# Kernel optimization log

Measured on AMD Instinct MI355X. Metric: run time of the kernel, lower is better.

Reference implementation:

```python
import jax, jax.numpy as jnp
import numpy as np

N_STATE = 1024
N_HEAD = 16
D_HEAD = N_STATE // N_HEAD  # 64
B, T = 4, 4096


def _linear(x, W, b=None):
    # x: (B,C,T,1), W: (O,C) == 1x1 conv2d over channel dim
    y = jnp.einsum('oc,bctx->botx', W, x)
    if b is not None:
        y = y + b[None, :, None, None]
    return y


def _phi(x):
    return jax.nn.silu(x) + 1.0


def setup_inputs() -> dict:
    key = jax.random.key(0)
    ks = jax.random.split(key, 8)
    s = 1.0 / np.sqrt(N_STATE).astype(np.float32)
    x = jax.random.normal(ks[0], (B, N_STATE, T, 1), jnp.float32)
    Wq = jax.random.normal(ks[1], (N_STATE, N_STATE), jnp.float32) * s
    bq = jax.random.normal(ks[2], (N_STATE,), jnp.float32) * s
    Wk = jax.random.normal(ks[3], (N_STATE, N_STATE), jnp.float32) * s
    Wv = jax.random.normal(ks[4], (N_STATE, N_STATE), jnp.float32) * s
    bv = jax.random.normal(ks[5], (N_STATE,), jnp.float32) * s
    Wo = jax.random.normal(ks[6], (N_STATE, N_STATE), jnp.float32) * s
    bo = jax.random.normal(ks[7], (N_STATE,), jnp.float32) * s
    return {"x": x, "Wq": Wq, "bq": bq, "Wk": Wk, "Wv": Wv, "bv": bv, "Wo": Wo, "bo": bo}


def reference(x, Wq, bq, Wk, Wv, bv, Wo, bo):
    Bb, C, Tt, _ = x.shape
    H, Dh = N_HEAD, D_HEAD
    q = _linear(x, Wq, bq)
    k = _linear(x, Wk)          # key has no bias
    v = _linear(x, Wv, bv)
    # (B, C, T, 1) -> (B, H, Dh, T, 1); C = H*Dh so reshape matches torch
    phi_q = _phi(q).reshape(Bb, H, Dh, Tt, 1)
    phi_k = _phi(k).reshape(Bb, H, Dh, Tt, 1)
    v = v.reshape(Bb, H, Dh, Tt, 1)
    k_sum = jnp.cumsum(phi_k, axis=3)
    kv_sum = jnp.cumsum(phi_k * v, axis=3)
    den = jnp.sum(phi_q * k_sum, axis=2, keepdims=True) + 1e-6
    out = (phi_q * kv_sum / den).reshape(Bb, C, Tt, 1)
    out = out / np.sqrt(Dh).astype(np.float32)
    return _linear(out, Wo, bo)
```

## Files before the change

### kernel.cpp

```cpp
#include <hip/hip_runtime.h>
#include <hip/hip_bf16.h>
#include <stdint.h>

#define T_SEQ 4096
#define C_ST  1024
#define K2    2048
#define K3    3072
#define NB    4
#define NCHUNK 128
#define CHUNK  32

typedef __bf16 bf16x8_t __attribute__((ext_vector_type(8)));
typedef float f32x4_t __attribute__((ext_vector_type(4)));
typedef unsigned short u16x8 __attribute__((ext_vector_type(8)));
typedef unsigned short u16x4 __attribute__((ext_vector_type(4)));
typedef __attribute__((address_space(1))) unsigned int as1u32;
typedef __attribute__((address_space(3))) unsigned int as3u32;

__device__ __forceinline__ unsigned short bfbits(float f) {
  __hip_bfloat16 h = __float2bfloat16(f);
  return *reinterpret_cast<unsigned short*>(&h);
}
__device__ __forceinline__ float bf2f(unsigned short u) {
  __hip_bfloat16 h;
  *reinterpret_cast<unsigned short*>(&h) = u;
  return __bfloat162float(h);
}
__device__ __forceinline__ float phi_f(float x) {
  return x / (1.0f + __expf(-x)) + 1.0f;
}

__global__ __launch_bounds__(256) void conv_w_kernel(
    const float* __restrict__ Wq, const float* __restrict__ Wk,
    const float* __restrict__ Wv, const float* __restrict__ Wo,
    unsigned short* __restrict__ W3, unsigned short* __restrict__ Wo3) {
  int r = blockIdx.x;
  int which = blockIdx.y;
  const float* src = (which == 0) ? Wq : (which == 1) ? Wk : (which == 2) ? Wv : Wo;
  unsigned short* dst = (which < 3) ? (W3 + (size_t)(which * 1024 + r) * K2)
                                    : (Wo3 + (size_t)r * K2);
  int c4 = threadIdx.x * 4;
  float4 v = *reinterpret_cast<const float4*>(&src[(size_t)r * 1024 + c4]);
  float fe[4] = {v.x, v.y, v.z, v.w};
  u16x4 hh;
#pragma unroll
  for (int e = 0; e < 4; ++e) hh[e] = bfbits(fe[e]);
  *reinterpret_cast<u16x4*>(&dst[c4])        = hh;
  *reinterpret_cast<u16x4*>(&dst[1024 + c4]) = hh;
}

__global__ __launch_bounds__(256) void conv_x_kernel(
    const float* __restrict__ x0, unsigned short* __restrict__ xT0) {
  __shared__ float tile[64][65];
  int c0 = blockIdx.y * 64, t0 = blockIdx.x * 64, z = blockIdx.z;
  const float* xb = x0 + (size_t)z * C_ST * T_SEQ + (size_t)c0 * T_SEQ + t0;
  unsigned short* xT = xT0 + (size_t)z * T_SEQ * K2;
  int tid = threadIdx.x;
#pragma unroll
  for (int p = 0; p < 4; ++p) {
    int idx = tid + p * 256;
    int r = idx >> 4, q4 = (idx & 15) * 4;
    float4 v = *reinterpret_cast<const float4*>(&xb[(size_t)r * T_SEQ + q4]);
    tile[r][q4 + 0] = v.x; tile[r][q4 + 1] = v.y;
    tile[r][q4 + 2] = v.z; tile[r][q4 + 3] = v.w;
  }
  __syncthreads();
  int r = tid >> 2, q = (tid & 3) * 16;
  u16x8 h0, h1, l0, l1;
#pragma unroll
  for (int j = 0; j < 8; ++j) {
    float f = tile[q + j][r];
    unsigned short hb = bfbits(f);
    h0[j] = hb; l0[j] = bfbits(f - bf2f(hb));
  }
#pragma unroll
  for (int j = 0; j < 8; ++j) {
    float f = tile[q + 8 + j][r];
    unsigned short hb = bfbits(f);
    h1[j] = hb; l1[j] = bfbits(f - bf2f(hb));
  }
  unsigned short* dst = xT + ((size_t)(t0 + r)) * K2 + c0 + q;
  *reinterpret_cast<u16x8*>(dst)         = h0;
  *reinterpret_cast<u16x8*>(dst + 8)     = h1;
  *reinterpret_cast<u16x8*>(dst + 1024)  = l0;
  *reinterpret_cast<u16x8*>(dst + 1032)  = l1;
}

__global__ __launch_bounds__(256) void gemm_bt_kernel(
    const unsigned short* __restrict__ A, const unsigned short* __restrict__ B,
    float* __restrict__ C, const float* __restrict__ biasM,
    int M, int N, int K, long long sA, long long sB, long long sC) {
  __shared__ unsigned short As[128 * 64];
  __shared__ unsigned short Bs[128 * 64];
  int z = blockIdx.z;
  const unsigned short* Ab = A + (size_t)z * sA;
  const unsigned short* Bb = B + (size_t)z * sB;
  float* Cb = C + (size_t)z * sC;
  int m0 = blockIdx.y * 128, n0 = blockIdx.x * 128;
  int tid = threadIdx.x, lane = tid & 63, wid = tid >> 6;
  int wr = wid >> 1, wc = wid & 1;
  int l16 = lane & 15, l4 = lane >> 4;
  int seg_src = (lane & 7) ^ ((lane >> 3) & 7);
  f32x4_t acc[4][4] = {};

  for (int k0 = 0; k0 < K; k0 += 64) {
    __syncthreads();
#pragma unroll
    for (int s = 0; s < 4; ++s) {
      int chunk = wid * 4 + s;
      int row = chunk * 8 + (lane >> 3);
      const unsigned short* ga = Ab + (size_t)(m0 + row) * K + k0 + seg_src * 8;
      const unsigned short* gb = Bb + (size_t)(n0 + row) * K + k0 + seg_src * 8;
      __builtin_amdgcn_global_load_lds((as1u32*)ga, (as3u32*)(As + chunk * 512), 16, 0, 0);
      __builtin_amdgcn_global_load_lds((as1u32*)gb, (as3u32*)(Bs + chunk * 512), 16, 0, 0);
    }
    __syncthreads();
#pragma unroll
    for (int s2 = 0; s2 < 2; ++s2) {
      bf16x8_t af[4], bfr[4];
      int kseg = s2 * 4 + l4;
#pragma unroll
      for (int m = 0; m < 4; ++m) {
        int r = wr * 64 + m * 16 + l16;
        af[m] = *reinterpret_cast<const bf16x8_t*>(&As[r * 64 + (kseg ^ (r & 7)) * 8]);
      }
#pragma unroll
      for (int n = 0; n < 4; ++n) {
        int r = wc * 64 + n * 16 + l16;
        bfr[n] = *reinterpret_cast<const bf16x8_t*>(&Bs[r * 64 + (kseg ^ (r & 7)) * 8]);
      }
#pragma unroll
      for (int m = 0; m < 4; ++m)
#pragma unroll
        for (int n = 0; n < 4; ++n)
          acc[m][n] = __builtin_amdgcn_mfma_f32_16x16x32_bf16(af[m], bfr[n], acc[m][n], 0, 0, 0);
    }
  }

#pragma unroll
  for (int m = 0; m < 4; ++m) {
#pragma unroll
    for (int n = 0; n < 4; ++n) {
      int row = m0 + wr * 64 + m * 16 + l4 * 4;
      int col = n0 + wc * 64 + n * 16 + l16;
#pragma unroll
      for (int j = 0; j < 4; ++j) {
        float val = acc[m][n][j];
        if (biasM) val += biasM[row + j];
        Cb[(size_t)(row + j) * N + col] = val;
      }
    }
  }
}

__global__ __launch_bounds__(256) void scan_a_kernel(
    const float* __restrict__ qkvT0, const float* __restrict__ bv,
    float* __restrict__ partK, float* __restrict__ partKV) {
  int d = threadIdx.x & 63;
  int w = threadIdx.x >> 6;
  int ch = blockIdx.x * 4 + w, h = blockIdx.y, z = blockIdx.z;
  int c = h * 64 + d;
  float bvc = bv[c];
  const float* base = qkvT0 + (size_t)z * T_SEQ * K3 + (size_t)ch * CHUNK * K3;
  float sk = 0.f, skv = 0.f;
  for (int tt = 0; tt < CHUNK; tt += 4) {
    float kv[4], vv[4];
#pragma unroll
    for (int u = 0; u < 4; ++u) {
      const float* row = base + (size_t)(tt + u) * K3;
      kv[u] = row[1024 + c];
      vv[u] = row[2048 + c];
    }
#pragma unroll
    for (int u = 0; u < 4; ++u) {
      float pk = phi_f(kv[u]);
      sk += pk; skv += pk * (vv[u] + bvc);
    }
  }
  size_t pidx = (((size_t)z * 16 + h) * NCHUNK + ch) * 64 + d;
  partK[pidx] = sk;
  partKV[pidx] = skv;
}

__global__ void scan_b_kernel(float* __restrict__ partK, float* __restrict__ partKV) {
  int d = threadIdx.x;
  int h = blockIdx.x, z = blockIdx.y;
  size_t base = ((size_t)z * 16 + h) * NCHUNK * 64 + d;
  float rk = 0.f, rkv = 0.f;
  for (int ch = 0; ch < NCHUNK; ++ch) {
    size_t i = base + (size_t)ch * 64;
    float tk = partK[i], tkv = partKV[i];
    partK[i] = rk; partKV[i] = rkv;
    rk += tk; rkv += tkv;
  }
}

__global__ __launch_bounds__(256) void scan_c_kernel(
    const float* __restrict__ qkvT0,
    const float* __restrict__ bq, const float* __restrict__ bv,
    const float* __restrict__ partK, const float* __restrict__ partKV,
    unsigned short* __restrict__ outT0) {
  int d = threadIdx.x & 63;
  int w = threadIdx.x >> 6;
  int ch = blockIdx.x * 4 + w, h = blockIdx.y, z = blockIdx.z;
  int c = h * 64 + d;
  size_t pidx = (((size_t)z * 16 + h) * NCHUNK + ch) * 64 + d;
  float sk = partK[pidx], skv = partKV[pidx];
  float bqc = bq[c], bvc = bv[c];
  const float* base = qkvT0 + (size_t)z * T_SEQ * K3 + (size_t)ch * CHUNK * K3;
  unsigned short* obase = outT0 + (size_t)z * T_SEQ * K2 + (size_t)ch * CHUNK * K2;
  for (int tt = 0; tt < CHUNK; tt += 4) {
    float qv[4], kv[4], vv[4];
#pragma unroll
    for (int u = 0; u < 4; ++u) {
      const float* row = base + (size_t)(tt + u) * K3;
      qv[u] = row[c];
      kv[u] = row[1024 + c];
      vv[u] = row[2048 + c];
    }
    float pq[4], dp[4], skv_s[4];
#pragma unroll
    for (int u = 0; u < 4; ++u) {
      pq[u] = phi_f(qv[u] + bqc);
      float pk = phi_f(kv[u]);
      sk += pk; skv += pk * (vv[u] + bvc);
      dp[u] = pq[u] * sk;
      skv_s[u] = skv;
    }
#pragma unroll
    for (int off = 32; off > 0; off >>= 1)
#pragma unroll
      for (int u = 0; u < 4; ++u) dp[u] += __shfl_xor(dp[u], off);
#pragma unroll
    for (int u = 0; u < 4; ++u) {
      float o = pq[u] * skv_s[u] / (dp[u] + 1e-6f) * 0.125f;
      unsigned short oh = bfbits(o);
      unsigned short ol = bfbits(o - bf2f(oh));
      unsigned short* orow = obase + (size_t)(tt + u) * K2;
      orow[c] = oh; orow[1024 + c] = ol;
    }
  }
}

extern "C" void kernel_launch(void* const* d_in, const int* in_sizes, int n_in,
                              void* d_out, int out_size, void* d_ws, size_t ws_size,
                              hipStream_t stream) {
  const float* x  = (const float*)d_in[0];
  const float* Wq = (const float*)d_in[1];
  const float* bq = (const float*)d_in[2];
  const float* Wk = (const float*)d_in[3];
  const float* Wv = (const float*)d_in[4];
  const float* bv = (const float*)d_in[5];
  const float* Wo = (const float*)d_in[6];
  const float* bo = (const float*)d_in[7];
  float* out = (float*)d_out;

  const size_t BASE = 16777216;
  const size_t PER  = 16777216ULL + 50331648ULL + 2 * 524288ULL;
  int PB = (ws_size >= BASE + 4 * PER) ? 4 : (ws_size >= BASE + 2 * PER) ? 2
         : (ws_size >= BASE + 1 * PER) ? 1 : 0;
  if (PB == 0) return;

  char* w = (char*)d_ws;
  unsigned short* W3     = (unsigned short*)(w);
  unsigned short* Wo3    = (unsigned short*)(w + 12582912);
  unsigned short* xT     = (unsigned short*)(w + BASE);
  float*          qkvT   = (float*)(w + BASE + (size_t)PB * 16777216);
  float*          partK  = (float*)(w + BASE + (size_t)PB * 67108864);
  float*          partKV = (float*)(w + BASE + (size_t)PB * 67108864 + (size_t)PB * 524288);

  conv_w_kernel<<<dim3(1024, 4), 256, 0, stream>>>(Wq, Wk, Wv, Wo, W3, Wo3);

  for (int g = 0; g < NB; g += PB) {
    const float* xg = x + (size_t)g * C_ST * T_SEQ;
    float* outg = out + (size_t)g * C_ST * T_SEQ;
    conv_x_kernel<<<dim3(T_SEQ / 64, C_ST / 64, PB), 256, 0, stream>>>(xg, xT);
    gemm_bt_kernel<<<dim3(K3 / 128, T_SEQ / 128, PB), 256, 0, stream>>>(
        xT, W3, qkvT, nullptr, T_SEQ, K3, K2,
        (long long)T_SEQ * K2, 0LL, (long long)T_SEQ * K3);
    scan_a_kernel<<<dim3(NCHUNK / 4, 16, PB), 256, 0, stream>>>(qkvT, bv, partK, partKV);
    scan_b_kernel<<<dim3(16, PB), 64, 0, stream>>>(partK, partKV);
    scan_c_kernel<<<dim3(NCHUNK / 4, 16, PB), 256, 0, stream>>>(qkvT, bq, bv, partK, partKV, xT);
    gemm_bt_kernel<<<dim3(T_SEQ / 128, C_ST / 128, PB), 256, 0, stream>>>(
        Wo3, xT, outg, bo, C_ST, T_SEQ, K2,
        0LL, (long long)T_SEQ * K2, (long long)C_ST * T_SEQ);
  }
}
```

Before: 581.1 us.

## Fuse bias and phi into QKV GEMM epilogue, store QKV as bf16

The QKV GEMM epilogue now adds the biases and applies phi to q and k, then writes the result as bf16 instead of fp32. This halves the intermediate traffic that both scan kernels read and drops the repeated phi evaluation from them. The scan loops are also unrolled to 8 timesteps. Storing phi(q), phi(k) and v in bf16 loses precision before the cumulative sums, which may hurt accuracy over long sequences.

```diff
diff --git a/kernel.cpp b/kernel.cpp
--- a/kernel.cpp
+++ b/kernel.cpp
@@ -88,14 +88,14 @@
 
 __global__ __launch_bounds__(256) void gemm_bt_kernel(
     const unsigned short* __restrict__ A, const unsigned short* __restrict__ B,
-    float* __restrict__ C, const float* __restrict__ biasM,
-    int M, int N, int K, long long sA, long long sB, long long sC) {
+    void* __restrict__ Cout, const float* __restrict__ biasRow,
+    const float* __restrict__ bq, const float* __restrict__ bv,
+    int M, int N, int K, long long sA, long long sB, long long sC, int mode) {
   __shared__ unsigned short As[128 * 64];
   __shared__ unsigned short Bs[128 * 64];
   int z = blockIdx.z;
   const unsigned short* Ab = A + (size_t)z * sA;
   const unsigned short* Bb = B + (size_t)z * sB;
-  float* Cb = C + (size_t)z * sC;
   int m0 = blockIdx.y * 128, n0 = blockIdx.x * 128;
   int tid = threadIdx.x, lane = tid & 63, wid = tid >> 6;
   int wr = wid >> 1, wc = wid & 1;
@@ -137,45 +137,57 @@
     }
   }
 
-#pragma unroll
-  for (int m = 0; m < 4; ++m) {
-#pragma unroll
-    for (int n = 0; n < 4; ++n) {
-      int row = m0 + wr * 64 + m * 16 + l4 * 4;
-      int col = n0 + wc * 64 + n * 16 + l16;
-#pragma unroll
-      for (int j = 0; j < 4; ++j) {
-        float val = acc[m][n][j];
-        if (biasM) val += biasM[row + j];
-        Cb[(size_t)(row + j) * N + col] = val;
-      }
-    }
+  if (mode == 0) {
+    float* Cb = (float*)Cout + (size_t)z * sC;
+#pragma unroll
+    for (int m = 0; m < 4; ++m)
+#pragma unroll
+      for (int n = 0; n < 4; ++n) {
+        int row = m0 + wr * 64 + m * 16 + l4 * 4;
+        int col = n0 + wc * 64 + n * 16 + l16;
+#pragma unroll
+        for (int j = 0; j < 4; ++j)
+          Cb[(size_t)(row + j) * N + col] = acc[m][n][j] + biasRow[row + j];
+      }
+  } else {
+    unsigned short* Cb = (unsigned short*)Cout + (size_t)z * sC;
+#pragma unroll
+    for (int m = 0; m < 4; ++m)
+#pragma unroll
+      for (int n = 0; n < 4; ++n) {
+        int row = m0 + wr * 64 + m * 16 + l4 * 4;
+        int col = n0 + wc * 64 + n * 16 + l16;
+#pragma unroll
+        for (int j = 0; j < 4; ++j) {
+          float val = acc[m][n][j];
+          if (col < 1024)       val = phi_f(val + bq[col]);
+          else if (col < 2048)  val = phi_f(val);
+          else                  val = val + bv[col - 2048];
+          Cb[(size_t)(row + j) * N + col] = bfbits(val);
+        }
+      }
   }
 }
 
 __global__ __launch_bounds__(256) void scan_a_kernel(
-    const float* __restrict__ qkvT0, const float* __restrict__ bv,
+    const unsigned short* __restrict__ qkv0,
     float* __restrict__ partK, float* __restrict__ partKV) {
   int d = threadIdx.x & 63;
   int w = threadIdx.x >> 6;
   int ch = blockIdx.x * 4 + w, h = blockIdx.y, z = blockIdx.z;
   int c = h * 64 + d;
-  float bvc = bv[c];
-  const float* base = qkvT0 + (size_t)z * T_SEQ * K3 + (size_t)ch * CHUNK * K3;
+  const unsigned short* base = qkv0 + (size_t)z * T_SEQ * K3 + (size_t)ch * CHUNK * K3;
   float sk = 0.f, skv = 0.f;
-  for (int tt = 0; tt < CHUNK; tt += 4) {
-    float kv[4], vv[4];
-#pragma unroll
-    for (int u = 0; u < 4; ++u) {
-      const float* row = base + (size_t)(tt + u) * K3;
-      kv[u] = row[1024 + c];
-      vv[u] = row[2048 + c];
-    }
-#pragma unroll
-    for (int u = 0; u < 4; ++u) {
-      float pk = phi_f(kv[u]);
-      sk += pk; skv += pk * (vv[u] + bvc);
-    }
+  for (int tt = 0; tt < CHUNK; tt += 8) {
+    float kt[8], vt[8];
+#pragma unroll
+    for (int u = 0; u < 8; ++u) {
+      const unsigned short* row = base + (size_t)(tt + u) * K3;
+      kt[u] = bf2f(row[1024 + c]);
+      vt[u] = bf2f(row[2048 + c]);
+    }
+#pragma unroll
+    for (int u = 0; u < 8; ++u) { sk += kt[u]; skv += kt[u] * vt[u]; }
   }
   size_t pidx = (((size_t)z * 16 + h) * NCHUNK + ch) * 64 + d;
   partK[pidx] = sk;
@@ -196,8 +208,7 @@
 }
 
 __global__ __launch_bounds__(256) void scan_c_kernel(
-    const float* __restrict__ qkvT0,
-    const float* __restrict__ bq, const float* __restrict__ bv,
+    const unsigned short* __restrict__ qkv0,
     const float* __restrict__ partK, const float* __restrict__ partKV,
     unsigned short* __restrict__ outT0) {
   int d = threadIdx.x & 63;
@@ -206,33 +217,30 @@
   int c = h * 64 + d;
   size_t pidx = (((size_t)z * 16 + h) * NCHUNK + ch) * 64 + d;
   float sk = partK[pidx], skv = partKV[pidx];
-  float bqc = bq[c], bvc = bv[c];
-  const float* base = qkvT0 + (size_t)z * T_SEQ * K3 + (size_t)ch * CHUNK * K3;
+  const unsigned short* base = qkv0 + (size_t)z * T_SEQ * K3 + (size_t)ch * CHUNK * K3;
   unsigned short* obase = outT0 + (size_t)z * T_SEQ * K2 + (size_t)ch * CHUNK * K2;
-  for (int tt = 0; tt < CHUNK; tt += 4) {
-    float qv[4], kv[4], vv[4];
-#pragma unroll
-    for (int u = 0; u < 4; ++u) {
-      const float* row = base + (size_t)(tt + u) * K3;
-      qv[u] = row[c];
-      kv[u] = row[1024 + c];
-      vv[u] = row[2048 + c];
-    }
-    float pq[4], dp[4], skv_s[4];
-#pragma unroll
-    for (int u = 0; u < 4; ++u) {
-      pq[u] = phi_f(qv[u] + bqc);
-      float pk = phi_f(kv[u]);
-      sk += pk; skv += pk * (vv[u] + bvc);
+  for (int tt = 0; tt < CHUNK; tt += 8) {
+    float pq[8], kt[8], vt[8];
+#pragma unroll
+    for (int u = 0; u < 8; ++u) {
+      const unsigned short* row = base + (size_t)(tt + u) * K3;
+      pq[u] = bf2f(row[c]);
+      kt[u] = bf2f(row[1024 + c]);
+      vt[u] = bf2f(row[2048 + c]);
+    }
+    float dp[8], skv_s[8];
+#pragma unroll
+    for (int u = 0; u < 8; ++u) {
+      sk += kt[u]; skv += kt[u] * vt[u];
       dp[u] = pq[u] * sk;
       skv_s[u] = skv;
     }
 #pragma unroll
     for (int off = 32; off > 0; off >>= 1)
 #pragma unroll
-      for (int u = 0; u < 4; ++u) dp[u] += __shfl_xor(dp[u], off);
-#pragma unroll
-    for (int u = 0; u < 4; ++u) {
+      for (int u = 0; u < 8; ++u) dp[u] += __shfl_xor(dp[u], off);
+#pragma unroll
+    for (int u = 0; u < 8; ++u) {
       float o = pq[u] * skv_s[u] / (dp[u] + 1e-6f) * 0.125f;
       unsigned short oh = bfbits(o);
       unsigned short ol = bfbits(o - bf2f(oh));
@@ -256,7 +264,7 @@
   float* out = (float*)d_out;
 
   const size_t BASE = 16777216;
-  const size_t PER  = 16777216ULL + 50331648ULL + 2 * 524288ULL;
+  const size_t PER  = 16777216ULL + 25165824ULL + 2 * 524288ULL;
   int PB = (ws_size >= BASE + 4 * PER) ? 4 : (ws_size >= BASE + 2 * PER) ? 2
          : (ws_size >= BASE + 1 * PER) ? 1 : 0;
   if (PB == 0) return;
@@ -265,9 +273,9 @@
   unsigned short* W3     = (unsigned short*)(w);
   unsigned short* Wo3    = (unsigned short*)(w + 12582912);
   unsigned short* xT     = (unsigned short*)(w + BASE);
-  float*          qkvT   = (float*)(w + BASE + (size_t)PB * 16777216);
-  float*          partK  = (float*)(w + BASE + (size_t)PB * 67108864);
-  float*          partKV = (float*)(w + BASE + (size_t)PB * 67108864 + (size_t)PB * 524288);
+  unsigned short* qkv    = (unsigned short*)(w + BASE + (size_t)PB * 16777216);
+  float*          partK  = (float*)(w + BASE + (size_t)PB * 41943040);
+  float*          partKV = (float*)(w + BASE + (size_t)PB * 41943040 + (size_t)PB * 524288);
 
   conv_w_kernel<<<dim3(1024, 4), 256, 0, stream>>>(Wq, Wk, Wv, Wo, W3, Wo3);
 
@@ -276,13 +284,13 @@
     float* outg = out + (size_t)g * C_ST * T_SEQ;
     conv_x_kernel<<<dim3(T_SEQ / 64, C_ST / 64, PB), 256, 0, stream>>>(xg, xT);
     gemm_bt_kernel<<<dim3(K3 / 128, T_SEQ / 128, PB), 256, 0, stream>>>(
-        xT, W3, qkvT, nullptr, T_SEQ, K3, K2,
-        (long long)T_SEQ * K2, 0LL, (long long)T_SEQ * K3);
-    scan_a_kernel<<<dim3(NCHUNK / 4, 16, PB), 256, 0, stream>>>(qkvT, bv, partK, partKV);
+        xT, W3, qkv, nullptr, bq, bv, T_SEQ, K3, K2,
+        (long long)T_SEQ * K2, 0LL, (long long)T_SEQ * K3, 1);
+    scan_a_kernel<<<dim3(NCHUNK / 4, 16, PB), 256, 0, stream>>>(qkv, partK, partKV);
     scan_b_kernel<<<dim3(16, PB), 64, 0, stream>>>(partK, partKV);
-    scan_c_kernel<<<dim3(NCHUNK / 4, 16, PB), 256, 0, stream>>>(qkvT, bq, bv, partK, partKV, xT);
+    scan_c_kernel<<<dim3(NCHUNK / 4, 16, PB), 256, 0, stream>>>(qkv, partK, partKV, xT);
     gemm_bt_kernel<<<dim3(T_SEQ / 128, C_ST / 128, PB), 256, 0, stream>>>(
-        Wo3, xT, outg, bo, C_ST, T_SEQ, K2,
-        0LL, (long long)T_SEQ * K2, (long long)C_ST * T_SEQ);
-  }
-}
+        Wo3, xT, outg, bo, nullptr, nullptr, C_ST, T_SEQ, K2,
+        0LL, (long long)T_SEQ * K2, (long long)C_ST * T_SEQ, 0);
+  }
+}
```

Result: slower. 596.3 us (+2.6%).
